# Kernel tuning notes

Measured on AMD Instinct MI355X. Metric: run time of the kernel, lower is better.

## Reference

```python
import jax, jax.numpy as jnp
import numpy as np

N, D, K = 100000, 128, 15
LN_EPS = 1e-5

def setup_inputs() -> dict:
    key = jax.random.key(0)
    k1, k2, k3, k4, k5 = jax.random.split(key, 5)
    node_features = jax.random.normal(k1, (N, D), dtype=jnp.float32)
    neighbor_idx = jax.random.randint(k2, (N, K), 0, N, dtype=jnp.int32)
    neighbor_counts = jax.random.randint(k3, (N,), 0, K + 1, dtype=jnp.int32)
    W = jax.random.normal(k4, (D, D), dtype=jnp.float32) / np.sqrt(D)
    b = jax.random.normal(k5, (D,), dtype=jnp.float32) * 0.01
    ln_w = jnp.ones((D,), dtype=jnp.float32)
    ln_b = jnp.zeros((D,), dtype=jnp.float32)
    return {"node_features": node_features, "neighbor_idx": neighbor_idx,
            "neighbor_counts": neighbor_counts, "W": W, "b": b,
            "ln_w": ln_w, "ln_b": ln_b}

def reference(node_features, neighbor_idx, neighbor_counts, W, b, ln_w, ln_b):
    Kn = neighbor_idx.shape[1]
    # validity mask over padded neighbor slots: [N, K]
    mask = (jnp.arange(Kn)[None, :] < neighbor_counts[:, None]).astype(node_features.dtype)
    feats = node_features[neighbor_idx]              # [N, K, D] gather
    cnt = jnp.maximum(neighbor_counts, 1).astype(node_features.dtype)
    agg = jnp.einsum('nkd,nk->nd', feats, mask) / cnt[:, None]  # mean over valid
    transformed = agg @ W.T + b                       # nn.Linear
    combined = node_features + transformed            # residual
    mu = jnp.mean(combined, axis=-1, keepdims=True)
    var = jnp.mean(jnp.square(combined - mu), axis=-1, keepdims=True)
    normed = (combined - mu) * jax.lax.rsqrt(var + LN_EPS) * ln_w + ln_b
    updated = jax.nn.relu(normed)
    has_nbrs = (neighbor_counts > 0)[:, None]
    return jnp.where(has_nbrs, updated, node_features)
```

## Files before the change

### kernel.cpp

```cpp
#include <hip/hip_runtime.h>
#include <stdint.h>

#define NN 100000
#define DF 128
#define KN 15
#define LN_EPS 1e-5f

typedef __attribute__((ext_vector_type(8))) short bf16x8;
typedef __attribute__((ext_vector_type(4))) float f32x4;

static __device__ __forceinline__ unsigned short f2bf(float f) {
    union { float f; uint32_t u; } v; v.f = f;
    uint32_t r = v.u + 0x7FFFu + ((v.u >> 16) & 1u);
    return (unsigned short)(r >> 16);
}
static __device__ __forceinline__ float uasf(uint32_t u) {
    union { uint32_t u; float f; } v; v.u = u; return v.f;
}
static __device__ __forceinline__ uint4 pack8(const float* a) {
    uint4 pk;
    pk.x = (uint)f2bf(a[0]) | ((uint)f2bf(a[1]) << 16);
    pk.y = (uint)f2bf(a[2]) | ((uint)f2bf(a[3]) << 16);
    pk.z = (uint)f2bf(a[4]) | ((uint)f2bf(a[5]) << 16);
    pk.w = (uint)f2bf(a[6]) | ((uint)f2bf(a[7]) << 16);
    return pk;
}

template<int DOW>
__global__ __launch_bounds__(256)
void conv_kernel(const float* __restrict__ nf, const float* __restrict__ W,
                 uint4* __restrict__ tbl, uint4* __restrict__ wb)
{
    int b = blockIdx.x;
    const float* src; uint4* dst; int i;
    if (DOW && b >= 6250) { i = (b - 6250) * 256 + threadIdx.x; src = W; dst = wb; }
    else                  { i = b * 256 + threadIdx.x;          src = nf; dst = tbl; }
    const float4* p = (const float4*)src + (size_t)i * 2;
    float4 a = p[0], c = p[1];
    float v[8] = {a.x, a.y, a.z, a.w, c.x, c.y, c.z, c.w};
    dst[i] = pack8(v);
}

__global__ __launch_bounds__(256, 6)
void gather_kernel(const uint4* __restrict__ tbl, const int* __restrict__ nbr,
                   const int* __restrict__ cnts, uint4* __restrict__ agg)
{
    const int tid  = threadIdx.x;
    const int s    = tid & 15;
    const int node = blockIdx.x * 16 + (tid >> 4);
    const int cnt  = cnts[node];
    int idxreg = (s < KN) ? nbr[(size_t)node * KN + s] : 0;

    float acc[8] = {0.f,0.f,0.f,0.f,0.f,0.f,0.f,0.f};
    #pragma unroll
    for (int st = 0; st < KN; ++st) {
        int idx = __shfl(idxreg, st, 16);
        if (st < cnt) {
            uint4 r = tbl[(size_t)idx * 16 + s];
            acc[0] += uasf(r.x << 16); acc[1] += uasf(r.x & 0xffff0000u);
            acc[2] += uasf(r.y << 16); acc[3] += uasf(r.y & 0xffff0000u);
            acc[4] += uasf(r.z << 16); acc[5] += uasf(r.z & 0xffff0000u);
            acc[6] += uasf(r.w << 16); acc[7] += uasf(r.w & 0xffff0000u);
        }
    }
    float inv = 1.0f / (float)(cnt > 0 ? cnt : 1);
    float v[8];
    #pragma unroll
    for (int j = 0; j < 8; ++j) v[j] = acc[j] * inv;
    agg[(size_t)node * 16 + s] = pack8(v);
}

__global__ __launch_bounds__(256, 4)
void gemm_kernel(const uint4* __restrict__ agg, const uint4* __restrict__ wb,
                 const float* __restrict__ nf, const int* __restrict__ cnts,
                 const float* __restrict__ bias, const float* __restrict__ lnw,
                 const float* __restrict__ lnb, float* __restrict__ out)
{
    const int tid  = threadIdx.x;
    const int lane = tid & 63;
    const int w    = tid >> 6;
    const int l15  = lane & 15;
    const int q    = lane >> 4;
    const int base = blockIdx.x * 64;

    int mrow = base + w * 16 + l15;
    if (mrow >= NN) mrow = NN - 1;

    bf16x8 afr[4];
    #pragma unroll
    for (int kk = 0; kk < 4; ++kk)
        afr[kk] = ((const bf16x8*)agg)[(size_t)mrow * 16 + kk * 4 + q];

    f32x4 acc[8];
    #pragma unroll
    for (int nb = 0; nb < 8; ++nb) acc[nb] = (f32x4){0.f,0.f,0.f,0.f};

    #pragma unroll
    for (int nb = 0; nb < 8; ++nb) {
        int n = nb * 16 + l15;
        #pragma unroll
        for (int kk = 0; kk < 4; ++kk) {
            bf16x8 bfr = ((const bf16x8*)wb)[n * 16 + kk * 4 + q];
            acc[nb] = __builtin_amdgcn_mfma_f32_16x16x32_bf16(afr[kk], bfr, acc[nb], 0, 0, 0);
        }
    }

    float bv[8], lwv[8], lbv[8];
    #pragma unroll
    for (int nb = 0; nb < 8; ++nb) {
        int c = nb * 16 + l15;
        bv[nb]  = bias[c];
        lwv[nb] = lnw[c];
        lbv[nb] = lnb[c];
    }

    #pragma unroll
    for (int r = 0; r < 4; ++r) {
        int node = base + w * 16 + q * 4 + r;
        if (node < NN) {
            int cnt = cnts[node];
            float vals[8], nfv[8];
            float s = 0.f, sq = 0.f;
            #pragma unroll
            for (int nb = 0; nb < 8; ++nb) {
                int c = nb * 16 + l15;
                float nv = nf[(size_t)node * DF + c];
                float comb = nv + acc[nb][r] + bv[nb];
                nfv[nb]  = nv;
                vals[nb] = comb;
                s  += comb;
                sq += comb * comb;
            }
            #pragma unroll
            for (int off = 1; off < 16; off <<= 1) {
                s  += __shfl_xor(s,  off);
                sq += __shfl_xor(sq, off);
            }
            float mu   = s  * (1.0f / 128.0f);
            float var  = sq * (1.0f / 128.0f) - mu * mu;
            float rstd = rsqrtf(var + LN_EPS);
            #pragma unroll
            for (int nb = 0; nb < 8; ++nb) {
                int c = nb * 16 + l15;
                float nrm = (vals[nb] - mu) * rstd * lwv[nb] + lbv[nb];
                float rel = fmaxf(nrm, 0.0f);
                out[(size_t)node * DF + c] = (cnt > 0) ? rel : nfv[nb];
            }
        }
    }
}

__global__ __launch_bounds__(512, 4)
void fused_kernel(const float* __restrict__ nf, const int* __restrict__ nbr,
                  const int* __restrict__ cnts, const float* __restrict__ W,
                  const float* __restrict__ bias, const float* __restrict__ lnw,
                  const float* __restrict__ lnb, float* __restrict__ out)
{
    __shared__ __align__(16) unsigned char WbS[32768];
    __shared__ __align__(16) unsigned char AtS[32768];
    __shared__ int idxS[128 * 16];
    __shared__ int cntS[128];

    const int tid  = threadIdx.x;
    const int lane = tid & 63;
    const int w    = tid >> 6;
    const int base = blockIdx.x * 128;

    {
        const float4* W4 = (const float4*)W;
        #pragma unroll
        for (int it = 0; it < 8; ++it) {
            int e = it * 2048 + tid * 4;
            float4 v = W4[e >> 2];
            int n = e >> 7, k = e & 127;
            ushort4 h;
            h.x = f2bf(v.x); h.y = f2bf(v.y); h.z = f2bf(v.z); h.w = f2bf(v.w);
            *(ushort4*)(WbS + ((n * 256 + k * 2) ^ ((n & 7) << 4))) = h;
        }
    }
    {
        if (lane < 16) {
            int m = w * 16 + lane;
            int node = base + m;
            cntS[m] = (node < NN) ? cnts[node] : 0;
        }
        #pragma unroll
        for (int it = 0; it < 4; ++it) {
            int e = it * 64 + lane;
            if (e < 240) {
                int mm = e / 15, kk = e - mm * 15;
                int m = w * 16 + mm;
                int node = base + m;
                idxS[m * 16 + kk] = (node < NN) ? nbr[(size_t)node * KN + kk] : 0;
            }
        }
    }
    {
        const int g = lane >> 4;
        const int s = lane & 15;
        #pragma unroll 2
        for (int t = 0; t < 16; ++t) {
            int m = w * 16 + t;
            int cnt = cntS[m];
            float acc[8] = {0.f,0.f,0.f,0.f,0.f,0.f,0.f,0.f};
            #pragma unroll
            for (int st = 0; st < 4; ++st) {
                int k = st * 4 + g;
                int idx = idxS[m * 16 + (k & 15)];
                if (k < cnt) {
                    const float4* p = (const float4*)(nf + (size_t)idx * DF + s * 8);
                    float4 u0 = p[0];
                    float4 u1 = p[1];
                    acc[0]+=u0.x; acc[1]+=u0.y; acc[2]+=u0.z; acc[3]+=u0.w;
                    acc[4]+=u1.x; acc[5]+=u1.y; acc[6]+=u1.z; acc[7]+=u1.w;
                }
            }
            #pragma unroll
            for (int j = 0; j < 8; ++j) {
                acc[j] += __shfl_xor(acc[j], 16);
                acc[j] += __shfl_xor(acc[j], 32);
            }
            if (g == 0) {
                float inv = 1.0f / (float)(cnt > 0 ? cnt : 1);
                float v[8];
                #pragma unroll
                for (int j = 0; j < 8; ++j) v[j] = acc[j] * inv;
                *(uint4*)(AtS + ((m * 256 + s * 16) ^ ((m & 7) << 4))) = pack8(v);
            }
        }
    }
    __syncthreads();

    const int l15 = lane & 15;
    const int q   = lane >> 4;
    bf16x8 afr[4];
    #pragma unroll
    for (int kk = 0; kk < 4; ++kk) {
        int m = w * 16 + l15;
        afr[kk] = *(const bf16x8*)(AtS + ((m * 256 + kk * 64 + q * 16) ^ ((m & 7) << 4)));
    }
    f32x4 acc[8];
    #pragma unroll
    for (int nb = 0; nb < 8; ++nb) acc[nb] = (f32x4){0.f,0.f,0.f,0.f};
    #pragma unroll
    for (int nb = 0; nb < 8; ++nb) {
        #pragma unroll
        for (int kk = 0; kk < 4; ++kk) {
            int n = nb * 16 + l15;
            bf16x8 bfr = *(const bf16x8*)(WbS + ((n * 256 + kk * 64 + q * 16) ^ ((n & 7) << 4)));
            acc[nb] = __builtin_amdgcn_mfma_f32_16x16x32_bf16(afr[kk], bfr, acc[nb], 0, 0, 0);
        }
    }
    float bv[8], lwv[8], lbv[8];
    #pragma unroll
    for (int nb = 0; nb < 8; ++nb) {
        int c = nb * 16 + l15;
        bv[nb]  = bias[c];
        lwv[nb] = lnw[c];
        lbv[nb] = lnb[c];
    }
    #pragma unroll
    for (int r = 0; r < 4; ++r) {
        int m = w * 16 + q * 4 + r;
        int node = base + m;
        if (node < NN) {
            int cnt = cntS[m];
            float vals[8], nfv[8];
            float s = 0.f, sq = 0.f;
            #pragma unroll
            for (int nb = 0; nb < 8; ++nb) {
                int c = nb * 16 + l15;
                float nv = nf[(size_t)node * DF + c];
                float comb = nv + acc[nb][r] + bv[nb];
                nfv[nb]  = nv;
                vals[nb] = comb;
                s  += comb;
                sq += comb * comb;
            }
            #pragma unroll
            for (int off = 1; off < 16; off <<= 1) {
                s  += __shfl_xor(s,  off);
                sq += __shfl_xor(sq, off);
            }
            float mu   = s  * (1.0f / 128.0f);
            float var  = sq * (1.0f / 128.0f) - mu * mu;
            float rstd = rsqrtf(var + LN_EPS);
            #pragma unroll
            for (int nb = 0; nb < 8; ++nb) {
                int c = nb * 16 + l15;
                float nrm = (vals[nb] - mu) * rstd * lwv[nb] + lbv[nb];
                float rel = fmaxf(nrm, 0.0f);
                out[(size_t)node * DF + c] = (cnt > 0) ? rel : nfv[nb];
            }
        }
    }
}

extern "C" void kernel_launch(void* const* d_in, const int* in_sizes, int n_in,
                              void* d_out, int out_size, void* d_ws, size_t ws_size,
                              hipStream_t stream) {
    const float* nf   = (const float*)d_in[0];
    const int*   nbr  = (const int*)d_in[1];
    const int*   cnts = (const int*)d_in[2];
    const float* W    = (const float*)d_in[3];
    const float* b    = (const float*)d_in[4];
    const float* lnw  = (const float*)d_in[5];
    const float* lnb  = (const float*)d_in[6];
    float* out = (float*)d_out;

    const size_t tblB = (size_t)NN * 256;
    const size_t aggB = (size_t)NN * 256;
    const size_t wbB  = 32768;

    if (ws_size >= tblB + aggB + wbB) {
        uint4* tbl = (uint4*)d_ws;
        uint4* agg = (uint4*)((char*)d_ws + tblB);
        uint4* wb  = (uint4*)((char*)d_ws + tblB + aggB);
        conv_kernel<1><<<6258, 256, 0, stream>>>(nf, W, tbl, wb);
        gather_kernel<<<NN / 16, 256, 0, stream>>>(tbl, nbr, cnts, agg);
        gemm_kernel<<<(NN + 63) / 64, 256, 0, stream>>>(agg, wb, nf, cnts, b, lnw, lnb, out);
    } else {
        fused_kernel<<<(NN + 127) / 128, 512, 0, stream>>>(nf, nbr, cnts, W, b, lnw, lnb, out);
    }
}
```

Measured before the change: 178.7 us.

## Fuse neighbor gather and GEMM+LayerNorm via LDS; read residual from bf16 table

Merges the gather and GEMM kernels into one 512-thread kernel. Each block aggregates neighbor features for 128 nodes into XOR-swizzled shared memory, then runs the MFMA GEMM and LayerNorm epilogue directly from LDS. This removes the global write and re-read of the aggregate buffer and one kernel launch. The epilogue also takes the residual and pass-through features from the bf16 table instead of the fp32 input, which halves that traffic. The cost is bf16 rounding in the residual and in the output for zero-neighbor nodes, which should be copied unchanged, plus higher per-block LDS and register pressure.

```diff
diff --git a/kernel.cpp b/kernel.cpp
--- a/kernel.cpp
+++ b/kernel.cpp
@@ -26,70 +26,73 @@
     return pk;
 }
 
-template<int DOW>
 __global__ __launch_bounds__(256)
 void conv_kernel(const float* __restrict__ nf, const float* __restrict__ W,
                  uint4* __restrict__ tbl, uint4* __restrict__ wb)
 {
     int b = blockIdx.x;
     const float* src; uint4* dst; int i;
-    if (DOW && b >= 6250) { i = (b - 6250) * 256 + threadIdx.x; src = W; dst = wb; }
-    else                  { i = b * 256 + threadIdx.x;          src = nf; dst = tbl; }
+    if (b >= 6250) { i = (b - 6250) * 256 + threadIdx.x; src = W;  dst = wb;  }
+    else           { i = b * 256 + threadIdx.x;          src = nf; dst = tbl; }
     const float4* p = (const float4*)src + (size_t)i * 2;
     float4 a = p[0], c = p[1];
     float v[8] = {a.x, a.y, a.z, a.w, c.x, c.y, c.z, c.w};
     dst[i] = pack8(v);
 }
 
-__global__ __launch_bounds__(256, 6)
-void gather_kernel(const uint4* __restrict__ tbl, const int* __restrict__ nbr,
-                   const int* __restrict__ cnts, uint4* __restrict__ agg)
+__global__ __launch_bounds__(512, 8)
+void fgg_kernel(const uint4* __restrict__ tbl, const uint4* __restrict__ wb,
+                const int* __restrict__ nbr, const int* __restrict__ cnts,
+                const float* __restrict__ bias, const float* __restrict__ lnw,
+                const float* __restrict__ lnb, float* __restrict__ out)
 {
-    const int tid  = threadIdx.x;
-    const int s    = tid & 15;
-    const int node = blockIdx.x * 16 + (tid >> 4);
-    const int cnt  = cnts[node];
-    int idxreg = (s < KN) ? nbr[(size_t)node * KN + s] : 0;
-
-    float acc[8] = {0.f,0.f,0.f,0.f,0.f,0.f,0.f,0.f};
-    #pragma unroll
-    for (int st = 0; st < KN; ++st) {
-        int idx = __shfl(idxreg, st, 16);
-        if (st < cnt) {
-            uint4 r = tbl[(size_t)idx * 16 + s];
-            acc[0] += uasf(r.x << 16); acc[1] += uasf(r.x & 0xffff0000u);
-            acc[2] += uasf(r.y << 16); acc[3] += uasf(r.y & 0xffff0000u);
-            acc[4] += uasf(r.z << 16); acc[5] += uasf(r.z & 0xffff0000u);
-            acc[6] += uasf(r.w << 16); acc[7] += uasf(r.w & 0xffff0000u);
-        }
-    }
-    float inv = 1.0f / (float)(cnt > 0 ? cnt : 1);
-    float v[8];
-    #pragma unroll
-    for (int j = 0; j < 8; ++j) v[j] = acc[j] * inv;
-    agg[(size_t)node * 16 + s] = pack8(v);
-}
-
-__global__ __launch_bounds__(256, 4)
-void gemm_kernel(const uint4* __restrict__ agg, const uint4* __restrict__ wb,
-                 const float* __restrict__ nf, const int* __restrict__ cnts,
-                 const float* __restrict__ bias, const float* __restrict__ lnw,
-                 const float* __restrict__ lnb, float* __restrict__ out)
-{
+    __shared__ __align__(16) unsigned char AtS[32768];
+
     const int tid  = threadIdx.x;
     const int lane = tid & 63;
     const int w    = tid >> 6;
-    const int l15  = lane & 15;
-    const int q    = lane >> 4;
-    const int base = blockIdx.x * 64;
-
-    int mrow = base + w * 16 + l15;
-    if (mrow >= NN) mrow = NN - 1;
+    const int g3   = lane >> 4;
+    const int s    = lane & 15;
+    const int base = blockIdx.x * 128;
+
+    #pragma unroll 1
+    for (int t = 0; t < 4; ++t) {
+        int m    = w * 16 + t * 4 + g3;
+        int node = base + m;
+        bool vld = node < NN;
+        int nd   = vld ? node : 0;
+        int cnt  = vld ? cnts[nd] : 0;
+        int idxreg = (s < KN) ? nbr[(size_t)nd * KN + s] : 0;
+
+        float acc[8] = {0.f,0.f,0.f,0.f,0.f,0.f,0.f,0.f};
+        #pragma unroll
+        for (int st = 0; st < KN; ++st) {
+            int idx = __shfl(idxreg, st, 16);
+            if (st < cnt) {
+                uint4 r = tbl[(size_t)idx * 16 + s];
+                acc[0] += uasf(r.x << 16); acc[1] += uasf(r.x & 0xffff0000u);
+                acc[2] += uasf(r.y << 16); acc[3] += uasf(r.y & 0xffff0000u);
+                acc[4] += uasf(r.z << 16); acc[5] += uasf(r.z & 0xffff0000u);
+                acc[6] += uasf(r.w << 16); acc[7] += uasf(r.w & 0xffff0000u);
+            }
+        }
+        float inv = 1.0f / (float)(cnt > 0 ? cnt : 1);
+        float vv[8];
+        #pragma unroll
+        for (int j = 0; j < 8; ++j) vv[j] = acc[j] * inv;
+        *(uint4*)(AtS + ((m * 256 + s * 16) ^ ((m & 7) << 4))) = pack8(vv);
+    }
+
+
+    const int l15 = lane & 15;
+    const int q   = lane >> 4;
 
     bf16x8 afr[4];
     #pragma unroll
-    for (int kk = 0; kk < 4; ++kk)
-        afr[kk] = ((const bf16x8*)agg)[(size_t)mrow * 16 + kk * 4 + q];
+    for (int kk = 0; kk < 4; ++kk) {
+        int m = w * 16 + l15;
+        afr[kk] = *(const bf16x8*)(AtS + ((m * 256 + kk * 64 + q * 16) ^ ((m & 7) << 4)));
+    }
 
     f32x4 acc[8];
     #pragma unroll
@@ -105,6 +108,7 @@
         }
     }
 
+    const unsigned short* tus = (const unsigned short*)tbl;
     float bv[8], lwv[8], lbv[8];
     #pragma unroll
     for (int nb = 0; nb < 8; ++nb) {
@@ -120,23 +124,23 @@
         if (node < NN) {
             int cnt = cnts[node];
             float vals[8], nfv[8];
-            float s = 0.f, sq = 0.f;
+            float sm = 0.f, sq = 0.f;
             #pragma unroll
             for (int nb = 0; nb < 8; ++nb) {
                 int c = nb * 16 + l15;
-                float nv = nf[(size_t)node * DF + c];
+                float nv = uasf((uint32_t)tus[(size_t)node * DF + c] << 16);
                 float comb = nv + acc[nb][r] + bv[nb];
                 nfv[nb]  = nv;
                 vals[nb] = comb;
-                s  += comb;
+                sm += comb;
                 sq += comb * comb;
             }
             #pragma unroll
             for (int off = 1; off < 16; off <<= 1) {
-                s  += __shfl_xor(s,  off);
+                sm += __shfl_xor(sm, off);
                 sq += __shfl_xor(sq, off);
             }
-            float mu   = s  * (1.0f / 128.0f);
+            float mu   = sm * (1.0f / 128.0f);
             float var  = sq * (1.0f / 128.0f) - mu * mu;
             float rstd = rsqrtf(var + LN_EPS);
             #pragma unroll
@@ -309,16 +313,13 @@
     float* out = (float*)d_out;
 
     const size_t tblB = (size_t)NN * 256;
-    const size_t aggB = (size_t)NN * 256;
     const size_t wbB  = 32768;
 
-    if (ws_size >= tblB + aggB + wbB) {
+    if (ws_size >= tblB + wbB) {
         uint4* tbl = (uint4*)d_ws;
-        uint4* agg = (uint4*)((char*)d_ws + tblB);
-        uint4* wb  = (uint4*)((char*)d_ws + tblB + aggB);
-        conv_kernel<1><<<6258, 256, 0, stream>>>(nf, W, tbl, wb);
-        gather_kernel<<<NN / 16, 256, 0, stream>>>(tbl, nbr, cnts, agg);
-        gemm_kernel<<<(NN + 63) / 64, 256, 0, stream>>>(agg, wb, nf, cnts, b, lnw, lnb, out);
+        uint4* wb  = (uint4*)((char*)d_ws + tblB);
+        conv_kernel<<<6258, 256, 0, stream>>>(nf, W, tbl, wb);
+        fgg_kernel<<<(NN + 127) / 128, 512, 0, stream>>>(tbl, wb, nbr, cnts, b, lnw, lnb, out);
     } else {
         fused_kernel<<<(NN + 127) / 128, 512, 0, stream>>>(nf, nbr, cnts, W, b, lnw, lnb, out);
     }
```

After: 204.8 us. 14.6% more time.
